# Kernel tuning notes

Measured on AMD Instinct MI355X. Metric: run time of the kernel, lower is better.

## Reference

```python
import jax, jax.numpy as jnp
import numpy as np

N_EMBD = 1024
N_HEAD = 16
D_K = N_EMBD // N_HEAD
B, T = 2, 2048
NEG = -10000000000.0


def setup_inputs() -> dict:
    key = jax.random.key(0)
    ks = jax.random.split(key, 9)
    s = 1.0 / np.sqrt(N_EMBD)
    mk = lambda k: jax.random.uniform(k, (N_EMBD, N_EMBD), jnp.float32, -s, s)
    mb = lambda k: jax.random.uniform(k, (N_EMBD,), jnp.float32, -s, s)
    return {
        "x": jax.random.normal(ks[0], (B, T, N_EMBD), jnp.float32),
        "Wq": mk(ks[1]), "bq": mb(ks[2]),
        "Wk": mk(ks[3]), "bk": mb(ks[4]),
        "Wv": mk(ks[5]), "bv": mb(ks[6]),
        "Wo": mk(ks[7]), "bo": mb(ks[8]),
    }


def reference(x, Wq, bq, Wk, bk, Wv, bv, Wo, bo):
    Bx, Tx, _ = x.shape
    split = lambda h: h.reshape(Bx, Tx, N_HEAD, D_K).transpose(0, 2, 1, 3)  # [B,H,T,d_k]
    q = split(x @ Wq.T + bq)
    k = split(x @ Wk.T + bk)
    v = split(x @ Wv.T + bv)
    scores = jnp.einsum("bhqd,bhkd->bhqk", q, k) / np.sqrt(D_K)
    causal = jnp.tril(jnp.ones((Tx, Tx), dtype=bool))
    scores = jnp.where(causal[None, None], scores, NEG)
    prob = jax.nn.softmax(scores, axis=-1)
    y = jnp.einsum("bhqk,bhkd->bhqd", prob, v)
    y = y.transpose(0, 2, 1, 3).reshape(Bx, Tx, N_EMBD)
    return y @ Wo.T + bo
```

## Files before the change

kernel.cpp:

```cpp
#include <hip/hip_runtime.h>
#include <hip/hip_bf16.h>

#define N_EMBD 1024
#define T_SEQ  2048
#define BATCH  2
#define NHEAD  16
#define DKH    64
#define MTOK   (BATCH * T_SEQ)

typedef __attribute__((ext_vector_type(8))) short short8;
typedef __attribute__((ext_vector_type(4))) short short4v;
typedef __attribute__((ext_vector_type(4))) float floatx4;

#define QSCALE 0.18033688011112042f

static __device__ __forceinline__ short bf16_of(float f) {
    union { float f; unsigned u; } x; x.f = f;
    unsigned r = (x.u + 0x7fff + ((x.u >> 16) & 1)) >> 16;
    return (short)r;
}

static __device__ __forceinline__ void gload16(const short* g, short* l) {
    __builtin_amdgcn_global_load_lds(
        (const __attribute__((address_space(1))) unsigned int*)(g),
        (__attribute__((address_space(3))) unsigned int*)(l),
        16, 0, 0);
}


__global__ __launch_bounds__(256) void cvt_frag(
    const float* __restrict__ x,  const float* __restrict__ Wq,
    const float* __restrict__ Wk, const float* __restrict__ Wv,
    const float* __restrict__ Wo,
    short* __restrict__ xf, short* __restrict__ wqkf,
    short* __restrict__ wvf, short* __restrict__ wof)
{
    int b = blockIdx.x;
    const float* src; short* dst; int srb, drb;
    if (b < 256)      { src = x;  dst = xf;   srb = b;       drb = srb; }
    else if (b < 320) { src = Wq; dst = wqkf; srb = b - 256; drb = srb; }
    else if (b < 384) { src = Wk; dst = wqkf; srb = b - 320; drb = srb + 64; }
    else if (b < 448) { src = Wv; dst = wvf;  srb = b - 384; drb = srb; }
    else              { src = Wo; dst = wof;  srb = b - 448; drb = srb; }

    const int row16 = threadIdx.x >> 4;
    const int kseg  = (threadIdx.x & 15) * 64;
    const float* sp = src + ((long)srb * 16 + row16) * 1024 + kseg;
    short* dp       = dst + ((long)drb * 32 + (kseg >> 5)) * 512 + row16 * 8;

#pragma unroll
    for (int c = 0; c < 8; ++c) {
        float4 v0 = *(const float4*)(sp + c * 8);
        float4 v1 = *(const float4*)(sp + c * 8 + 4);
        short8 o;
        o[0] = bf16_of(v0.x); o[1] = bf16_of(v0.y); o[2] = bf16_of(v0.z); o[3] = bf16_of(v0.w);
        o[4] = bf16_of(v1.x); o[5] = bf16_of(v1.y); o[6] = bf16_of(v1.z); o[7] = bf16_of(v1.w);
        *(short8*)(dp + (c >> 2) * 512 + (c & 3) * 128) = o;
    }
}

#define LDS_KLOOP(AfP, BfP, rb0, cb0)                                           \
    __shared__ short lds[3][16 * 512];                                          \
    floatx4 acc[4][4] = {};                                                     \
    {                                                                           \
        const int w_    = threadIdx.x >> 6;                                     \
        const int lane_ = threadIdx.x & 63;                                     \
        const int wr_   = w_ >> 1, wc_ = w_ & 1;                                \
        const short* gb = (w_ < 2                                               \
            ? (AfP) + (long)((rb0) + w_ * 4) * 32 * 512                         \
            : (BfP) + (long)((cb0) + (w_ - 2) * 4) * 32 * 512) + lane_ * 8;     \
        short* p0 = &lds[0][w_ * 4 * 512];                                      \
        short* p1 = &lds[1][w_ * 4 * 512];                                      \
        short* p2 = &lds[2][w_ * 4 * 512];                                      \
        const int lo_a = (wr_ * 4) * 512 + lane_ * 8 - w_ * 4 * 512;            \
        const int lo_b = (8 + wc_ * 4) * 512 + lane_ * 8 - w_ * 4 * 512;        \
        _Pragma("unroll") for (int f = 0; f < 4; ++f)                           \
            gload16(gb + (long)f * 32 * 512, p0 + f * 512);                     \
        _Pragma("unroll") for (int f = 0; f < 4; ++f)                           \
            gload16(gb + ((long)f * 32 + 1) * 512, p1 + f * 512);               \
        for (int kb = 0; kb < 32; ++kb) {                                       \
            if (kb < 31) asm volatile("s_waitcnt vmcnt(4)" ::: "memory");       \
            else         asm volatile("s_waitcnt vmcnt(0)" ::: "memory");       \
            __syncthreads();                                                    \
            if (kb + 2 < 32) {                                                  \
                _Pragma("unroll") for (int f = 0; f < 4; ++f)                   \
                    gload16(gb + ((long)f * 32 + kb + 2) * 512, p2 + f * 512);  \
            }                                                                   \
            short8 a_[4], b_[4];                                                \
            _Pragma("unroll") for (int i = 0; i < 4; ++i)                       \
                a_[i] = *(const short8*)(p0 + lo_a + i * 512);                  \
            _Pragma("unroll") for (int j = 0; j < 4; ++j)                       \
                b_[j] = *(const short8*)(p0 + lo_b + j * 512);                  \
            _Pragma("unroll") for (int i = 0; i < 4; ++i)                       \
                _Pragma("unroll") for (int j = 0; j < 4; ++j)                   \
                    acc[i][j] = __builtin_amdgcn_mfma_f32_16x16x32_bf16(        \
                        a_[i], b_[j], acc[i][j], 0, 0, 0);                      \
            short* t_ = p0; p0 = p1; p1 = p2; p2 = t_;                          \
        }                                                                       \
    }

__global__ __launch_bounds__(256) void gemm_qkv(
    const short* __restrict__ xf, const short* __restrict__ wqkf,
    const short* __restrict__ wvf,
    const float* __restrict__ bq, const float* __restrict__ bk, const float* __restrict__ bv,
    short* __restrict__ outQ, short* __restrict__ outK, short* __restrict__ outV)
{
    const int lane = threadIdx.x & 63;
    const int w    = threadIdx.x >> 6;
    const int quad = lane >> 4, lr = lane & 15;
    const int wr   = w >> 1, wc = w & 1;

    const int bid  = blockIdx.x;
    const bool isQK = bid < 512;
    int mt, nt;
    const short *Af, *Bf;
    if (isQK) { mt = bid >> 5;        nt = bid & 31; Af = wqkf; Bf = xf; }
    else      { int v = bid - 512;
                mt = v >> 3;          nt = v & 7;    Af = xf;   Bf = wvf; }

    const int rb0 = mt * 8;
    const int cb0 = nt * 8;
    const int mwv = mt * 128 + wr * 64;
    const int nwv = nt * 128 + wc * 64;

    LDS_KLOOP(Af, Bf, rb0, cb0)

    if (isQK) {
#pragma unroll
        for (int i = 0; i < 4; ++i) {
#pragma unroll
            for (int j = 0; j < 4; ++j) {
                int f0  = mwv + i * 16 + quad * 4;
                int t   = nwv + j * 16 + lr;
                int tb  = t & 2047;
                int sel = f0 >> 10;
                int fb  = f0 & 1023;
                int h   = fb >> 6, d0 = fb & 63;
                long bh = (long)(t >> 11) * NHEAD + h;
                float4 bias = *(const float4*)((sel ? bk : bq) + fb);
                short4v y;
#pragma unroll
                for (int r = 0; r < 4; ++r) {
                    float v = acc[i][j][r] + (&bias.x)[r];
                    if (sel == 0) v *= QSCALE;
                    y[r] = bf16_of(v);
                }
                long idx = ((bh * 128 + (tb >> 4)) * 2 + (d0 >> 5)) * 512
                         + (((d0 >> 3) & 3) * 16 + (tb & 15)) * 8 + (d0 & 7);
                *(short4v*)((sel ? outK : outQ) + idx) = y;
            }
        }
    } else {
#pragma unroll
        for (int i = 0; i < 4; ++i) {
#pragma unroll
            for (int j = 0; j < 4; ++j) {
                int t0 = mwv + i * 16 + quad * 4;
                int tb = t0 & 2047;
                int d  = nwv + j * 16 + lr;
                int h  = d >> 6, dblk = (d >> 4) & 3;
                long bh = (long)(t0 >> 11) * NHEAD + h;
                float bias = bv[d];
                short4v y;
#pragma unroll
                for (int r = 0; r < 4; ++r) y[r] = bf16_of(acc[i][j][r] + bias);
                long idx = ((bh * 64 + (tb >> 5)) * 4 + dblk) * 512
                         + lane * 8 + (i & 1) * 4;
                *(short4v*)(outV + idx) = y;
            }
        }
    }
}

__global__ __launch_bounds__(256) void gemm_proj(
    const short* __restrict__ Yf, const short* __restrict__ wof,
    const float* __restrict__ bo, float* __restrict__ out)
{
    const int lane = threadIdx.x & 63;
    const int w    = threadIdx.x >> 6;
    const int quad = lane >> 4, lr = lane & 15;
    const int wr   = w >> 1, wc = w & 1;

    const int bid = blockIdx.x;
    const int mt  = bid >> 5;
    const int nt  = bid & 31;

    const int rb0 = mt * 8;
    const int cb0 = nt * 8;
    const int mwv = mt * 128 + wr * 64;
    const int nwv = nt * 128 + wc * 64;

    LDS_KLOOP(wof, Yf, rb0, cb0)

#pragma unroll
    for (int i = 0; i < 4; ++i) {
#pragma unroll
        for (int j = 0; j < 4; ++j) {
            int  f0 = mwv + i * 16 + quad * 4;
            long t  = nwv + j * 16 + lr;
            float4 b4 = *(const float4*)(bo + f0);
            float4 o4;
            o4.x = acc[i][j][0] + b4.x;
            o4.y = acc[i][j][1] + b4.y;
            o4.z = acc[i][j][2] + b4.z;
            o4.w = acc[i][j][3] + b4.w;
            *(float4*)(out + t * N_EMBD + f0) = o4;
        }
    }
}

__global__ __launch_bounds__(256) void attn_kernel(
    const short* __restrict__ Qf, const short* __restrict__ Kf,
    const short* __restrict__ Vf, short* __restrict__ Y)
{
    __shared__ float Ob[2][32][68];
    __shared__ float Lb[2][32];

    const int tid  = threadIdx.x;
    const int w    = tid >> 6, lane = tid & 63;
    const int quad = lane >> 4, lr = lane & 15;
    const int qs   = w & 1, half = w >> 1;

    const int id = blockIdx.x;
    const int qt = 31 - (id >> 5);
    const int bh = id & 31;

    const short* Qp = Qf + (long)bh * 131072;
    const short* Kp = Kf + (long)bh * 131072;
    const short* Vp = Vf + (long)bh * 131072;

    const int qrb = qt * 64 + qs * 32;
    const int qb  = qrb >> 4;

    short8 qfv[2][2];
#pragma unroll
    for (int m = 0; m < 2; ++m)
#pragma unroll
        for (int c = 0; c < 2; ++c)
            qfv[m][c] = *(const short8*)(Qp + (long)(((qb + m) * 2 + c) * 512) + lane * 8);

    floatx4 o[2][4] = {};
    float rs[2] = {0.f, 0.f};

    const int S_tot = 2 * qt + qs + 1;
    const int h0 = (S_tot + 1) >> 1;
    const int sb = half ? h0 : 0;
    const int se = half ? S_tot : h0;

    short8 kbn[2][2];
    short8 vbn[4];
    if (sb < se) {
#pragma unroll
        for (int blk = 0; blk < 2; ++blk)
#pragma unroll
            for (int c = 0; c < 2; ++c)
                kbn[blk][c] = *(const short8*)(Kp + (long)(((sb * 2 + blk) * 2 + c) * 512) + lane * 8);
#pragma unroll
        for (int d = 0; d < 4; ++d)
            vbn[d] = *(const short8*)(Vp + (long)((sb * 4 + d) * 512) + lane * 8);
    }

    for (int s = sb; s < se; ++s) {
        short8 ka[2][2];
        short8 va[4];
#pragma unroll
        for (int blk = 0; blk < 2; ++blk)
#pragma unroll
            for (int c = 0; c < 2; ++c) ka[blk][c] = kbn[blk][c];
#pragma unroll
        for (int d = 0; d < 4; ++d) va[d] = vbn[d];

        if (s + 1 < se) {
#pragma unroll
            for (int blk = 0; blk < 2; ++blk)
#pragma unroll
                for (int c = 0; c < 2; ++c)
                    kbn[blk][c] = *(const short8*)(Kp + (long)((((s + 1) * 2 + blk) * 2 + c) * 512) + lane * 8);
#pragma unroll
            for (int d = 0; d < 4; ++d)
                vbn[d] = *(const short8*)(Vp + (long)(((s + 1) * 4 + d) * 512) + lane * 8);
        }

        floatx4 sc[2][2];
        __builtin_amdgcn_s_setprio(1);
#pragma unroll
        for (int m = 0; m < 2; ++m)
#pragma unroll
            for (int blk = 0; blk < 2; ++blk) {
                floatx4 z = {};
                z = __builtin_amdgcn_mfma_f32_16x16x32_bf16(ka[blk][0], qfv[m][0], z, 0, 0, 0);
                z = __builtin_amdgcn_mfma_f32_16x16x32_bf16(ka[blk][1], qfv[m][1], z, 0, 0, 0);
                sc[m][blk] = z;
            }
        __builtin_amdgcn_s_setprio(0);

        if (s == S_tot - 1) {
            const int k0 = s * 32;
#pragma unroll
            for (int m = 0; m < 2; ++m)
#pragma unroll
                for (int blk = 0; blk < 2; ++blk)
#pragma unroll
                    for (int r = 0; r < 4; ++r) {
                        int key = k0 + blk * 16 + quad * 4 + r;
                        if (key > qrb + m * 16 + lr) sc[m][blk][r] = -INFINITY;
                    }
        }

        short8 pa[2];
#pragma unroll
        for (int m = 0; m < 2; ++m) {
            union { short8 v; short e[8]; } pu;
#pragma unroll
            for (int blk = 0; blk < 2; ++blk)
#pragma unroll
                for (int r = 0; r < 4; ++r) {
                    float p = __builtin_amdgcn_exp2f(sc[m][blk][r]);
                    rs[m] += p;
                    union { float f; unsigned u; } cc; cc.f = p;
                    pu.e[blk * 4 + r] = (short)((cc.u + 0x8000u) >> 16);
                }
            pa[m] = pu.v;
        }

        __builtin_amdgcn_s_setprio(1);
#pragma unroll
        for (int m = 0; m < 2; ++m)
#pragma unroll
            for (int d = 0; d < 4; ++d)
                o[m][d] = __builtin_amdgcn_mfma_f32_16x16x32_bf16(va[d], pa[m], o[m][d], 0, 0, 0);
        __builtin_amdgcn_s_setprio(0);
    }

#pragma unroll
    for (int m = 0; m < 2; ++m) {
        rs[m] += __shfl_xor(rs[m], 16, 64);
        rs[m] += __shfl_xor(rs[m], 32, 64);
    }

    if (half == 1) {
#pragma unroll
        for (int m = 0; m < 2; ++m) {
#pragma unroll
            for (int d = 0; d < 4; ++d)
                *(floatx4*)&Ob[qs][m * 16 + lr][d * 16 + quad * 4] = o[m][d];
            Lb[qs][m * 16 + lr] = rs[m];
        }
    }
    __syncthreads();
    if (half == 0) {
        const long rb0 = (long)(bh >> 4) * 128 + qb;
        const int  hk  = (bh & 15) * DKH;
#pragma unroll
        for (int m = 0; m < 2; ++m) {
            float l   = rs[m] + Lb[qs][m * 16 + lr];
            float inv = 1.f / l;
            long  rb  = rb0 + m;
#pragma unroll
            for (int d = 0; d < 4; ++d) {
                floatx4 ob = *(const floatx4*)&Ob[qs][m * 16 + lr][d * 16 + quad * 4];
                short4v y4;
#pragma unroll
                for (int r = 0; r < 4; ++r) y4[r] = bf16_of((o[m][d][r] + ob[r]) * inv);
                int kb = hk + d * 16 + quad * 4;
                long idx = (rb * 32 + (kb >> 5)) * 512
                         + (((kb >> 3) & 3) * 16 + lr) * 8 + (quad & 1) * 4;
                *(short4v*)(Y + idx) = y4;
            }
        }
    }
}

extern "C" void kernel_launch(void* const* d_in, const int* in_sizes, int n_in,
                              void* d_out, int out_size, void* d_ws, size_t ws_size,
                              hipStream_t stream) {
    const float* x  = (const float*)d_in[0];
    const float* Wq = (const float*)d_in[1];
    const float* bq = (const float*)d_in[2];
    const float* Wk = (const float*)d_in[3];
    const float* bk = (const float*)d_in[4];
    const float* Wv = (const float*)d_in[5];
    const float* bv = (const float*)d_in[6];
    const float* Wo = (const float*)d_in[7];
    const float* bo = (const float*)d_in[8];
    float* out = (float*)d_out;

    char* ws = (char*)d_ws;
    short* xf   = (short*)(ws);
    short* wqkf = (short*)(ws + (8L  << 20));
    short* wvf  = (short*)(ws + (12L << 20));
    short* wof  = (short*)(ws + (14L << 20));
    short* Qb   = (short*)(ws + (16L << 20));
    short* Kbuf = (short*)(ws + (24L << 20));
    short* Vtb  = (short*)(ws + (32L << 20));
    short* Yf   = xf;

    cvt_frag<<<512, 256, 0, stream>>>(x, Wq, Wk, Wv, Wo, xf, wqkf, wvf, wof);

    gemm_qkv<<<768, 256, 0, stream>>>(xf, wqkf, wvf, bq, bk, bv, Qb, Kbuf, Vtb);
    attn_kernel<<<1024, 256, 0, stream>>>(Qb, Kbuf, Vtb, Yf);
    gemm_proj<<<256, 256, 0, stream>>>(Yf, wof, bo, out);
}
```

Measured before the change: 178.2 us.

## Replace LDS-tiled output projection with single-wave register GEMM; load V per step

The output projection GEMM moves from 256-thread blocks with a triple-buffered LDS k-loop to one wave per block. Each wave computes a 64x128 tile, loading pre-fragmented operands straight from global memory into registers with double buffering. This drops LDS staging and barriers, but loses operand sharing between waves and raises register pressure (128 accumulator registers). Separately, the attention kernel stops prefetching V one step ahead and loads it in the current iteration, which cuts live registers but exposes more load latency.

```diff
diff --git a/kernel.cpp b/kernel.cpp
--- a/kernel.cpp
+++ b/kernel.cpp
@@ -58,6 +58,34 @@
         *(short8*)(dp + (c >> 2) * 512 + (c & 3) * 128) = o;
     }
 }
+
+#define GEMM_KLOOP(Ab, Bb)                                                     \
+    floatx4 acc[4][8] = {};                                                    \
+    short8 a0[4], a1[4], b0[8], b1[8];                                         \
+    _Pragma("unroll") for (int i = 0; i < 4; ++i)                              \
+        a0[i] = *(const short8*)(Ab + (long)i * 32 * 512);                     \
+    _Pragma("unroll") for (int j = 0; j < 8; ++j)                              \
+        b0[j] = *(const short8*)(Bb + (long)j * 32 * 512);                     \
+    for (int kc = 0; kc < 32; kc += 2) {                                       \
+        _Pragma("unroll") for (int i = 0; i < 4; ++i)                          \
+            a1[i] = *(const short8*)(Ab + ((long)i * 32 + kc + 1) * 512);      \
+        _Pragma("unroll") for (int j = 0; j < 8; ++j)                          \
+            b1[j] = *(const short8*)(Bb + ((long)j * 32 + kc + 1) * 512);      \
+        _Pragma("unroll") for (int i = 0; i < 4; ++i)                          \
+            _Pragma("unroll") for (int j = 0; j < 8; ++j)                      \
+                acc[i][j] = __builtin_amdgcn_mfma_f32_16x16x32_bf16(           \
+                    a0[i], b0[j], acc[i][j], 0, 0, 0);                         \
+        if (kc + 2 < 32) {                                                     \
+            _Pragma("unroll") for (int i = 0; i < 4; ++i)                      \
+                a0[i] = *(const short8*)(Ab + ((long)i * 32 + kc + 2) * 512);  \
+            _Pragma("unroll") for (int j = 0; j < 8; ++j)                      \
+                b0[j] = *(const short8*)(Bb + ((long)j * 32 + kc + 2) * 512);  \
+        }                                                                      \
+        _Pragma("unroll") for (int i = 0; i < 4; ++i)                          \
+            _Pragma("unroll") for (int j = 0; j < 8; ++j)                      \
+                acc[i][j] = __builtin_amdgcn_mfma_f32_16x16x32_bf16(           \
+                    a1[i], b1[j], acc[i][j], 0, 0, 0);                         \
+    }
 
 #define LDS_KLOOP(AfP, BfP, rb0, cb0)                                           \
     __shared__ short lds[3][16 * 512];                                          \
@@ -172,32 +200,27 @@
     }
 }
 
-__global__ __launch_bounds__(256) void gemm_proj(
+__global__ __launch_bounds__(64, 2) void gemm_proj(
     const short* __restrict__ Yf, const short* __restrict__ wof,
     const float* __restrict__ bo, float* __restrict__ out)
 {
     const int lane = threadIdx.x & 63;
-    const int w    = threadIdx.x >> 6;
     const int quad = lane >> 4, lr = lane & 15;
-    const int wr   = w >> 1, wc = w & 1;
-
-    const int bid = blockIdx.x;
-    const int mt  = bid >> 5;
-    const int nt  = bid & 31;
-
-    const int rb0 = mt * 8;
-    const int cb0 = nt * 8;
-    const int mwv = mt * 128 + wr * 64;
-    const int nwv = nt * 128 + wc * 64;
-
-    LDS_KLOOP(wof, Yf, rb0, cb0)
+    const int wid  = blockIdx.x;
+    const int mw   = (wid >> 5) * 64;
+    const int nw   = (wid & 31) * 128;
+
+    const short* Ab = wof + (long)(mw >> 4) * 32 * 512 + lane * 8;
+    const short* Bb = Yf  + (long)(nw >> 4) * 32 * 512 + lane * 8;
+
+    GEMM_KLOOP(Ab, Bb)
 
 #pragma unroll
     for (int i = 0; i < 4; ++i) {
 #pragma unroll
-        for (int j = 0; j < 4; ++j) {
-            int  f0 = mwv + i * 16 + quad * 4;
-            long t  = nwv + j * 16 + lr;
+        for (int j = 0; j < 8; ++j) {
+            int  f0 = mw + i * 16 + quad * 4;
+            long t  = nw + j * 16 + lr;
             float4 b4 = *(const float4*)(bo + f0);
             float4 o4;
             o4.x = acc[i][j][0] + b4.x;
@@ -248,38 +271,31 @@
     const int se = half ? S_tot : h0;
 
     short8 kbn[2][2];
-    short8 vbn[4];
     if (sb < se) {
 #pragma unroll
         for (int blk = 0; blk < 2; ++blk)
 #pragma unroll
             for (int c = 0; c < 2; ++c)
                 kbn[blk][c] = *(const short8*)(Kp + (long)(((sb * 2 + blk) * 2 + c) * 512) + lane * 8);
-#pragma unroll
-        for (int d = 0; d < 4; ++d)
-            vbn[d] = *(const short8*)(Vp + (long)((sb * 4 + d) * 512) + lane * 8);
     }
 
     for (int s = sb; s < se; ++s) {
         short8 ka[2][2];
-        short8 va[4];
 #pragma unroll
         for (int blk = 0; blk < 2; ++blk)
 #pragma unroll
             for (int c = 0; c < 2; ++c) ka[blk][c] = kbn[blk][c];
-#pragma unroll
-        for (int d = 0; d < 4; ++d) va[d] = vbn[d];
-
         if (s + 1 < se) {
 #pragma unroll
             for (int blk = 0; blk < 2; ++blk)
 #pragma unroll
                 for (int c = 0; c < 2; ++c)
                     kbn[blk][c] = *(const short8*)(Kp + (long)((((s + 1) * 2 + blk) * 2 + c) * 512) + lane * 8);
-#pragma unroll
-            for (int d = 0; d < 4; ++d)
-                vbn[d] = *(const short8*)(Vp + (long)(((s + 1) * 4 + d) * 512) + lane * 8);
-        }
+        }
+        short8 va[4];
+#pragma unroll
+        for (int d = 0; d < 4; ++d)
+            va[d] = *(const short8*)(Vp + (long)((s * 4 + d) * 512) + lane * 8);
 
         floatx4 sc[2][2];
         __builtin_amdgcn_s_setprio(1);
@@ -399,5 +415,5 @@
 
     gemm_qkv<<<768, 256, 0, stream>>>(xf, wqkf, wvf, bq, bk, bv, Qb, Kbuf, Vtb);
     attn_kernel<<<1024, 256, 0, stream>>>(Qb, Kbuf, Vtb, Yf);
-    gemm_proj<<<256, 256, 0, stream>>>(Yf, wof, bo, out);
-}
+    gemm_proj<<<512, 64, 0, stream>>>(Yf, wof, bo, out);
+}
```

New measurement: 178.7 us. No clear change (+0.3%).
